# Optimization experiments

Measured on AMD Instinct MI355X. Metric: run time of the kernel, lower is better.

The kernel has to match this reference:

```python
import jax, jax.numpy as jnp
import numpy as np

A_COEF, B_COEF, C_COEF = 1.0, 0.1, 10.0
KL_COEF = 0.005
EPS = 1e-6

B, P1, F, P2 = 32, 778, 1538, 3000
PARAM_DIM, LATENT = 61, 64


def setup_inputs() -> dict:
    key = jax.random.key(0)
    ks = jax.random.split(key, 9)
    return {
        "recon_x": jax.random.normal(ks[0], (B, PARAM_DIM), jnp.float32),
        "x": jax.random.normal(ks[1], (B, PARAM_DIM), jnp.float32),
        "mu": jax.random.normal(ks[2], (B, LATENT), jnp.float32),
        "logvar": jax.random.normal(ks[3], (B, LATENT), jnp.float32),
        "recon_xyz": jax.random.normal(ks[4], (B, P1, 3), jnp.float32),
        "hand_xyz": jax.random.normal(ks[5], (B, P1, 3), jnp.float32),
        "hand_faces": jax.random.randint(ks[6], (B, F, 3), 0, P1, jnp.int64),
        "obj_pts": jax.random.normal(ks[7], (B, P2, 3), jnp.float32),
        "v_weights": jax.random.uniform(ks[8], (P1,), jnp.float32),
    }


def _verts_normals_single(verts, faces):
    # verts: (V,3), faces: (F,3). PyTorch3D-style area-weighted vertex normals.
    v0 = verts[faces[:, 0]]
    v1 = verts[faces[:, 1]]
    v2 = verts[faces[:, 2]]
    fn = jnp.cross(v1 - v0, v2 - v0)  # (F,3) ~ 2*area*face_normal
    n = (jnp.zeros_like(verts)
         .at[faces[:, 0]].add(fn)
         .at[faces[:, 1]].add(fn)
         .at[faces[:, 2]].add(fn))
    norm = jnp.linalg.norm(n, axis=-1, keepdims=True)
    return n / jnp.maximum(norm, EPS)


_verts_normals = jax.vmap(_verts_normals_single)


def _sqdist(xp, yp):
    # (B,P1,P2) pairwise squared distances
    x2 = jnp.sum(xp * xp, axis=-1)[:, :, None]
    y2 = jnp.sum(yp * yp, axis=-1)[:, None, :]
    return x2 + y2 - 2.0 * jnp.einsum('bpd,bqd->bpq', xp, yp)


def _point2point_signed(xp, yp, x_normals):
    # xp: (B,P1,3) hand, yp: (B,P2,3) object, x_normals: (B,P1,3)
    d2 = _sqdist(xp, yp)
    xidx = jnp.argmin(d2, axis=2)  # (B,P1) nearest object point per hand vert
    yidx = jnp.argmin(d2, axis=1)  # (B,P2) nearest hand vert per object point
    x_near = jnp.take_along_axis(yp, xidx[..., None], axis=1)  # (B,P1,3)
    y_near = jnp.take_along_axis(xp, yidx[..., None], axis=1)  # (B,P2,3)
    x2y = xp - x_near
    y2x = yp - y_near
    y_nn = jnp.take_along_axis(x_normals, yidx[..., None], axis=1)  # (B,P2,3)
    in_out = jnp.sign(jnp.sum(y_nn * y2x, axis=-1))
    y2x_signed = jnp.linalg.norm(y2x, axis=2) * in_out  # (B,P2)
    x2y_signed = jnp.linalg.norm(x2y, axis=2)           # (B,P1)
    return y2x_signed, x2y_signed


def _loss_cnet(verts_rhand, verts_rhand_gt, faces, verts_obj, v_weights):
    v_w2 = jnp.power(v_weights, 1.0 / 2.5)
    rh_n = _verts_normals(verts_rhand, faces)
    rh_n_gt = _verts_normals(verts_rhand_gt, faces)
    o2h, h2o = _point2point_signed(verts_rhand, verts_obj, rh_n)
    o2h_gt, h2o_gt = _point2point_signed(verts_rhand_gt, verts_obj, rh_n_gt)
    w_dist = (o2h_gt < 0.01) & (o2h_gt > -0.005)
    w_neg = o2h < 0.0
    w = jnp.where(w_neg, 1.5, jnp.where(w_dist, 1.0, 0.1))
    loss_h = 35.0 * (1.0 - KL_COEF) * jnp.mean(jnp.abs(jnp.abs(h2o) - jnp.abs(h2o_gt)) * v_w2)
    loss_o = 30.0 * (1.0 - KL_COEF) * jnp.mean(jnp.abs(o2h - o2h_gt) * w)
    return loss_h + loss_o


def reference(recon_x, x, mu, logvar, recon_xyz, hand_xyz, hand_faces, obj_pts, v_weights):
    bsz = recon_x.shape[0]
    param_loss = jnp.sum((recon_x - x) ** 2) / bsz
    recon_loss = jnp.sum((recon_xyz - hand_xyz) ** 2) / hand_xyz.shape[0]
    KLD = -0.5 * jnp.sum(1.0 + logvar - mu ** 2 - jnp.exp(logvar)) / hand_xyz.shape[0]
    cvae_loss = recon_loss + KLD
    ho_loss = _loss_cnet(recon_xyz, hand_xyz, hand_faces, obj_pts, v_weights)
    loss = A_COEF * cvae_loss + B_COEF * param_loss + C_COEF * ho_loss
    return loss, param_loss, ho_loss, recon_loss, KLD
```

## Files before the change

### kernel.cpp

```cpp
#include <hip/hip_runtime.h>
#include <math.h>

#define B 32
#define P1 778
#define NF 1538
#define P2 3000
#define PARAM_DIM 61
#define LATENT 64

#define P1PAD 784
#define NTH 49
#define CHO 768
#define NTO 12
#define NPART 16

#define RED1_BLKS 16
#define HC_BLKS 128
#define OC_BLKS 192
#define HALF_F 769

#define D1_NRM 128
#define D1_TOT (D1_NRM + RED1_BLKS)
#define D2_TOT 256
#define D3_TOT (OC_BLKS + HC_BLKS)

#define NP_OFF  0
#define NP_SZ   (2*2*B*P1*4)
#define OS_OFF  (NP_OFF + NP_SZ)
#define OS_SZ   (2*B*P2)
#define HP_OFF  (OS_OFF + OS_SZ)
#define HP_SZ   (NPART*2*B*P1PAD)
#define R1_OFF  (HP_OFF + HP_SZ)
#define RH_OFF  (R1_OFF + RED1_BLKS*3)
#define RO_OFF  (RH_OFF + HC_BLKS)

typedef __attribute__((ext_vector_type(8))) short bf16x8;
typedef __attribute__((ext_vector_type(4))) float f32x4;
union U4 { uint4 u; bf16x8 v; };

static __device__ __forceinline__ unsigned umin2(unsigned a, unsigned b) { return a < b ? a : b; }
static __device__ __forceinline__ unsigned bhi(float x) { return __float_as_uint(x) >> 16; }
static __device__ __forceinline__ float bres(float x, unsigned h) { return x - __uint_as_float(h << 16); }

__global__ __launch_bounds__(256) void kd1(
    const float* __restrict__ recon_x, const float* __restrict__ x,
    const float* __restrict__ mu, const float* __restrict__ logvar,
    const float* __restrict__ recon_xyz, const float* __restrict__ hand_xyz,
    const int* __restrict__ faces, float* __restrict__ ws) {
  __shared__ float4 sv[P1];
  __shared__ float sn[4][2336];
  const int tid = threadIdx.x;
  const int bid = blockIdx.x;

  if (bid < D1_NRM) {
    const int half = bid >> 6, r = bid & 63, set = r >> 5, b = r & 31;
    const float* verts = (set == 0 ? recon_xyz : hand_xyz) + b * P1 * 3;
    const int* f = faces + b * NF * 3 + half * HALF_F * 3;
    const int nf = (half == 0) ? HALF_F : (NF - HALF_F);
    for (int i = tid; i < P1; i += 256)
      sv[i] = make_float4(verts[3*i], verts[3*i+1], verts[3*i+2], 0.f);
    for (int i = tid; i < 4 * 2336; i += 256) ((float*)sn)[i] = 0.f;
    __syncthreads();
    float* s = sn[tid >> 6];
    for (int k = tid; k < nf; k += 256) {
      int i0 = f[3*k], i1 = f[3*k+1], i2 = f[3*k+2];
      float4 v0 = sv[i0], v1 = sv[i1], v2 = sv[i2];
      float e0x = v1.x - v0.x, e0y = v1.y - v0.y, e0z = v1.z - v0.z;
      float e1x = v2.x - v0.x, e1y = v2.y - v0.y, e1z = v2.z - v0.z;
      float fx = e0y * e1z - e0z * e1y;
      float fy = e0z * e1x - e0x * e1z;
      float fz = e0x * e1y - e0y * e1x;
      atomicAdd(&s[3*i0+0], fx); atomicAdd(&s[3*i0+1], fy); atomicAdd(&s[3*i0+2], fz);
      atomicAdd(&s[3*i1+0], fx); atomicAdd(&s[3*i1+1], fy); atomicAdd(&s[3*i1+2], fz);
      atomicAdd(&s[3*i2+0], fx); atomicAdd(&s[3*i2+1], fy); atomicAdd(&s[3*i2+2], fz);
    }
    __syncthreads();
    float4* np = (float4*)(ws + NP_OFF) + (size_t)((half * 2 + set) * B + b) * P1;
    for (int p = tid; p < P1; p += 256) {
      float nx = sn[0][3*p] + sn[1][3*p] + sn[2][3*p] + sn[3][3*p];
      float ny = sn[0][3*p+1] + sn[1][3*p+1] + sn[2][3*p+1] + sn[3][3*p+1];
      float nz = sn[0][3*p+2] + sn[1][3*p+2] + sn[2][3*p+2] + sn[3][3*p+2];
      np[p] = make_float4(nx, ny, nz, 0.f);
    }
  } else {
    const int blk = bid - D1_NRM;
    const int gtid = blk * 256 + tid, stride = RED1_BLKS * 256;
    float sp = 0.f, sr = 0.f, sk = 0.f;
    for (int i = gtid; i < B * PARAM_DIM; i += stride) { float d = recon_x[i] - x[i]; sp += d * d; }
    for (int i = gtid; i < B * P1 * 3; i += stride)    { float d = recon_xyz[i] - hand_xyz[i]; sr += d * d; }
    for (int i = gtid; i < B * LATENT; i += stride)    { float lv = logvar[i], m = mu[i]; sk += 1.f + lv - m * m - expf(lv); }
    for (int off = 32; off > 0; off >>= 1) {
      sp += __shfl_down(sp, off, 64);
      sr += __shfl_down(sr, off, 64);
      sk += __shfl_down(sk, off, 64);
    }
    float* sred = (float*)sn;
    const int wv = tid >> 6;
    if ((tid & 63) == 0) { sred[wv*3] = sp; sred[wv*3+1] = sr; sred[wv*3+2] = sk; }
    __syncthreads();
    if (tid == 0) {
      float a = 0.f, bb = 0.f, c = 0.f;
      for (int w = 0; w < 4; ++w) { a += sred[w*3]; bb += sred[w*3+1]; c += sred[w*3+2]; }
      ws[R1_OFF + blk*3+0] = a; ws[R1_OFF + blk*3+1] = bb; ws[R1_OFF + blk*3+2] = c;
    }
  }
}

__global__ __launch_bounds__(256, 1) void kd2(
    const float* __restrict__ recon_xyz, const float* __restrict__ hand_xyz,
    const float* __restrict__ obj, float* __restrict__ ws) {
  __shared__ float4 sVerts[P1PAD];
  __shared__ float4 sObj[CHO];
  __shared__ uint4  sPack4[(NTH + 1) * 32];
  __shared__ unsigned sKeys[CHO];
  __shared__ uint4  sZero;

  const int tid = threadIdx.x;
  const int bid = blockIdx.x;
  const int chunk = bid >> 6, rr = bid & 63, set = rr >> 5, b = rr & 31;
  const float* verts = (set == 0 ? recon_xyz : hand_xyz) + b * P1 * 3;
  const float* op = obj + (size_t)b * P2 * 3;

  if (tid == 0) sZero = make_uint4(0u, 0u, 0u, 0u);
  for (int i = tid; i < P1PAD; i += 256) {
    float vx, vy, vz;
    if (i < P1) { vx = verts[3*i]; vy = verts[3*i+1]; vz = verts[3*i+2]; }
    else        { vx = vy = vz = 1.0e6f; }
    sVerts[i] = make_float4(vx, vy, vz, 0.f);
  }
  for (int i = tid; i < CHO; i += 256) {
    const int q = chunk * CHO + i;
    float ox, oy, oz;
    if (q < P2) { ox = op[3*q]; oy = op[3*q+1]; oz = op[3*q+2]; }
    else        { ox = oy = oz = 1.0e6f; }
    sObj[i] = make_float4(ox, oy, oz, ox*ox + oy*oy + oz*oz);
  }
  __syncthreads();

  for (int idx = tid; idx < NTH * 32; idx += 256) {
    const int t = idx >> 5, vl = idx & 31, vg = vl >> 4;
    const float4 v = sVerts[t * 16 + (vl & 15)];
    const float sx = -2.f * v.x, sy = -2.f * v.y, sz = -2.f * v.z;
    const unsigned hx = bhi(sx), hy = bhi(sy), hz = bhi(sz);
    unsigned w0, w1, w2, w3;
    if (vg == 0) {
      const unsigned lx = bhi(bres(sx, hx));
      const unsigned ly = bhi(bres(sy, hy));
      const unsigned lz = bhi(bres(sz, hz));
      w0 = hx | (hy << 16);
      w1 = hz | (lx << 16);
      w2 = ly | (lz << 16);
      w3 = hx | (hy << 16);
    } else {
      const float h2 = v.x*v.x + v.y*v.y + v.z*v.z;
      const unsigned h2h = bhi(h2);
      const unsigned h2l = bhi(bres(h2, h2h));
      w0 = hz  | (h2h << 16);
      w1 = h2l | (0x3F80u << 16);
      w2 = 0x3F80u;
      w3 = 0u;
    }
    sPack4[t * 32 + vl] = make_uint4(w0, w1, w2, w3);
  }

  const int l = tid & 63, wv = tid >> 6, g = l >> 4, cl = l & 15;
  U4 bw[NTO];
  #pragma unroll
  for (int j = 0; j < NTO; ++j) {
    const float4 o = sObj[wv * 192 + j * 16 + cl];
    unsigned u0 = 0u, u1 = 0u, u2 = 0u, u3 = 0u;
    if (g == 0) {
      const unsigned ohx = bhi(o.x), ohy = bhi(o.y), ohz = bhi(o.z);
      const unsigned olx = bhi(bres(o.x, ohx));
      const unsigned oly = bhi(bres(o.y, ohy));
      u0 = ohx | (ohy << 16);
      u1 = ohz | (ohx << 16);
      u2 = ohy | (ohz << 16);
      u3 = olx | (oly << 16);
    } else if (g == 1) {
      const unsigned ohz = bhi(o.z);
      const unsigned olz = bhi(bres(o.z, ohz));
      const float o2p = o.w + 1.0f;
      const unsigned o2h = bhi(o2p);
      const unsigned o2l = bhi(bres(o2p, o2h));
      u0 = olz | (0x3F80u << 16);
      u1 = 0x3F80u | (o2h << 16);
      u2 = o2l;
      u3 = 0u;
    }
    bw[j].u = make_uint4(u0, u1, u2, u3);
  }
  __syncthreads();

  unsigned om[NTO];
  #pragma unroll
  for (int j = 0; j < NTO; ++j) om[j] = 0xFFFFFFFFu;

  float* hpart = ws + HP_OFF + (size_t)(((chunk * 4 + wv) * 2 + set) * B + b) * P1PAD;
  const f32x4 czero = {0.f, 0.f, 0.f, 0.f};

  const uint4* ap = (l < 32) ? ((const uint4*)sPack4 + l) : &sZero;
  const int astep = (l < 32) ? 32 : 0;
  uint4 au = *ap; ap += astep;

  int ib = g * 4;
  for (int t = 0; t < NTH; ++t, ib += 16) {
    const uint4 aunx = *ap; ap += astep;
    U4 ac; ac.u = au;
    float hm0 = 3.0e38f, hm1 = 3.0e38f, hm2 = 3.0e38f, hm3 = 3.0e38f;
    #pragma unroll
    for (int j = 0; j < NTO; ++j) {
      const f32x4 d = __builtin_amdgcn_mfma_f32_16x16x32_bf16(ac.v, bw[j].v, czero, 0, 0, 0);
      hm0 = fminf(hm0, d[0]); hm1 = fminf(hm1, d[1]);
      hm2 = fminf(hm2, d[2]); hm3 = fminf(hm3, d[3]);
      const unsigned k0 = (__float_as_uint(d[0]) & 0xFFFFFC00u) | (unsigned)(ib + 0);
      const unsigned k1 = (__float_as_uint(d[1]) & 0xFFFFFC00u) | (unsigned)(ib + 1);
      const unsigned k2 = (__float_as_uint(d[2]) & 0xFFFFFC00u) | (unsigned)(ib + 2);
      const unsigned k3 = (__float_as_uint(d[3]) & 0xFFFFFC00u) | (unsigned)(ib + 3);
      om[j] = umin2(om[j], umin2(umin2(k0, k1), umin2(k2, k3)));
    }
    #pragma unroll
    for (int m = 1; m <= 8; m <<= 1) {
      hm0 = fminf(hm0, __shfl_xor(hm0, m, 64));
      hm1 = fminf(hm1, __shfl_xor(hm1, m, 64));
      hm2 = fminf(hm2, __shfl_xor(hm2, m, 64));
      hm3 = fminf(hm3, __shfl_xor(hm3, m, 64));
    }
    if (cl == 0)
      *(float4*)&hpart[ib] = make_float4(hm0 - 1.f, hm1 - 1.f, hm2 - 1.f, hm3 - 1.f);
    au = aunx;
  }

  #pragma unroll
  for (int j = 0; j < NTO; ++j) {
    unsigned v = umin2(om[j], (unsigned)__shfl_xor((int)om[j], 16, 64));
    v = umin2(v, (unsigned)__shfl_xor((int)v, 32, 64));
    if (l < 16) sKeys[wv * 192 + j * 16 + l] = v;
  }
  __syncthreads();

  const float4* np0 = (const float4*)(ws + NP_OFF) + (size_t)(set * B + b) * P1;
  const float4* np1 = np0 + (size_t)2 * B * P1;
  float* os = ws + OS_OFF + (size_t)(set * B + b) * P2;
  for (int i = tid; i < CHO; i += 256) {
    const int q = chunk * CHO + i;
    if (q < P2) {
      const unsigned key = sKeys[i];
      int hi = (int)(key & 1023u); if (hi > P1 - 1) hi = P1 - 1;
      const float4 h = sVerts[hi];
      const float4 o = sObj[i];
      const float dx = o.x - h.x, dy = o.y - h.y, dz = o.z - h.z;
      const float d2 = fmaf(dx, dx, fmaf(dy, dy, dz * dz));
      const float4 na = np0[hi], nb = np1[hi];
      const float nx = na.x + nb.x, ny = na.y + nb.y, nz = na.z + nb.z;
      const float dt = nx * dx + ny * dy + nz * dz;
      const float sg = (dt > 0.f) ? 1.f : ((dt < 0.f) ? -1.f : 0.f);
      os[q] = sqrtf(d2) * sg;
    }
  }
}

__global__ __launch_bounds__(256) void kd3(const float* __restrict__ vw,
                                           float* __restrict__ ws) {
  __shared__ float sred[4];
  const int tid = threadIdx.x;
  const int bid = blockIdx.x;
  if (bid < OC_BLKS) {
    const int gtid = bid * 256 + tid, stride = OC_BLKS * 256;
    float so = 0.f;
    for (int i = gtid; i < B * P2; i += stride) {
      float osA = ws[OS_OFF + i];
      float osB = ws[OS_OFF + (size_t)B * P2 + i];
      bool wdist = (osB < 0.01f) && (osB > -0.005f);
      float w = (osA < 0.f) ? 1.5f : (wdist ? 1.f : 0.1f);
      so += fabsf(osA - osB) * w;
    }
    for (int off = 32; off > 0; off >>= 1) so += __shfl_down(so, off, 64);
    if ((tid & 63) == 0) sred[tid >> 6] = so;
    __syncthreads();
    if (tid == 0) ws[RO_OFF + bid] = sred[0] + sred[1] + sred[2] + sred[3];
  } else {
    const int blk = bid - OC_BLKS;
    const int gtid = blk * 256 + tid, stride = HC_BLKS * 256;
    float sh = 0.f;
    for (int i = gtid; i < B * P1; i += stride) {
      const int p = i % P1, bb = i / P1;
      const size_t base0 = (size_t)HP_OFF + (size_t)bb * P1PAD + p;
      float m0 = 3.0e38f, m1 = 3.0e38f;
      #pragma unroll
      for (int c = 0; c < NPART; ++c) {
        m0 = fminf(m0, ws[base0 + (size_t)(c*2+0) * B * P1PAD]);
        m1 = fminf(m1, ws[base0 + (size_t)(c*2+1) * B * P1PAD]);
      }
      m0 = fmaxf(m0, 0.f); m1 = fmaxf(m1, 0.f);
      sh += fabsf(sqrtf(m0) - sqrtf(m1)) * powf(vw[p], 0.4f);
    }
    for (int off = 32; off > 0; off >>= 1) sh += __shfl_down(sh, off, 64);
    if ((tid & 63) == 0) sred[tid >> 6] = sh;
    __syncthreads();
    if (tid == 0) ws[RH_OFF + blk] = sred[0] + sred[1] + sred[2] + sred[3];
  }
}

__global__ void kfin(const float* __restrict__ ws, float* __restrict__ out) {
  const int lane = threadIdx.x;
  float sp = 0.f, sr = 0.f, sk = 0.f, sh = 0.f, so = 0.f;
  for (int i = lane; i < RED1_BLKS; i += 64) {
    sp += ws[R1_OFF + i*3+0]; sr += ws[R1_OFF + i*3+1]; sk += ws[R1_OFF + i*3+2];
  }
  for (int i = lane; i < HC_BLKS; i += 64) sh += ws[RH_OFF + i];
  for (int i = lane; i < OC_BLKS; i += 64) so += ws[RO_OFF + i];
  for (int off = 32; off > 0; off >>= 1) {
    sp += __shfl_down(sp, off, 64);
    sr += __shfl_down(sr, off, 64);
    sk += __shfl_down(sk, off, 64);
    sh += __shfl_down(sh, off, 64);
    so += __shfl_down(so, off, 64);
  }
  if (lane == 0) {
    float param_loss = sp / (float)B;
    float recon_loss = sr / (float)B;
    float KLD = -0.5f * sk / (float)B;
    float cvae = recon_loss + KLD;
    float loss_h = 35.f * (1.f - 0.005f) * sh / (float)(B * P1);
    float loss_o = 30.f * (1.f - 0.005f) * so / (float)(B * P2);
    float ho = loss_h + loss_o;
    out[0] = cvae + 0.1f * param_loss + 10.f * ho;
    out[1] = param_loss;
    out[2] = ho;
    out[3] = recon_loss;
    out[4] = KLD;
  }
}

extern "C" void kernel_launch(void* const* d_in, const int* in_sizes, int n_in,
                              void* d_out, int out_size, void* d_ws, size_t ws_size,
                              hipStream_t stream) {
  const float* recon_x   = (const float*)d_in[0];
  const float* x         = (const float*)d_in[1];
  const float* mu        = (const float*)d_in[2];
  const float* logvar    = (const float*)d_in[3];
  const float* recon_xyz = (const float*)d_in[4];
  const float* hand_xyz  = (const float*)d_in[5];
  const int*   faces     = (const int*)d_in[6];
  const float* obj       = (const float*)d_in[7];
  const float* vw        = (const float*)d_in[8];
  float* ws = (float*)d_ws;
  float* out = (float*)d_out;

  kd1<<<dim3(D1_TOT), 256, 0, stream>>>(recon_x, x, mu, logvar,
                                        recon_xyz, hand_xyz, faces, ws);
  kd2<<<dim3(D2_TOT), 256, 0, stream>>>(recon_xyz, hand_xyz, obj, ws);
  kd3<<<dim3(D3_TOT), 256, 0, stream>>>(vw, ws);
  kfin<<<1, 64, 0, stream>>>(ws, out);
}
```

Baseline: 137.6 us.

## Split kd2 work so each wave covers a strided subset of hand tiles

Each kd2 block now handles 192 object points instead of 768, so the grid grows to 16 chunks × 64. Within a block the four waves share the same object tile and each takes every fourth hand tile. Per-wave keys are merged in shared memory. The shared vertex array is dropped and vertices are read directly from global memory, which cuts LDS use enough to allow 4 blocks per CU. The hand partial-min layout changes to one slice per chunk (16 partials), matching NPART. The aim is more blocks and more occupancy at the cost of repeating hand packing per block and extra global vertex gathers.

Measured after the change: 124.1 us. 9.8% less time.

```diff
diff --git a/kernel.cpp b/kernel.cpp
--- a/kernel.cpp
+++ b/kernel.cpp
@@ -10,8 +10,9 @@
 
 #define P1PAD 784
 #define NTH 49
-#define CHO 768
+#define CHO 192
 #define NTO 12
+#define NCH 16
 #define NPART 16
 
 #define RED1_BLKS 16
@@ -21,7 +22,7 @@
 
 #define D1_NRM 128
 #define D1_TOT (D1_NRM + RED1_BLKS)
-#define D2_TOT 256
+#define D2_TOT (NCH * 64)
 #define D3_TOT (OC_BLKS + HC_BLKS)
 
 #define NP_OFF  0
@@ -106,13 +107,12 @@
   }
 }
 
-__global__ __launch_bounds__(256, 1) void kd2(
+__global__ __launch_bounds__(256, 4) void kd2(
     const float* __restrict__ recon_xyz, const float* __restrict__ hand_xyz,
     const float* __restrict__ obj, float* __restrict__ ws) {
-  __shared__ float4 sVerts[P1PAD];
   __shared__ float4 sObj[CHO];
-  __shared__ uint4  sPack4[(NTH + 1) * 32];
-  __shared__ unsigned sKeys[CHO];
+  __shared__ uint4  sPack4[(NTH + 4) * 32];
+  __shared__ unsigned sKeys[4][CHO];
   __shared__ uint4  sZero;
 
   const int tid = threadIdx.x;
@@ -122,12 +122,6 @@
   const float* op = obj + (size_t)b * P2 * 3;
 
   if (tid == 0) sZero = make_uint4(0u, 0u, 0u, 0u);
-  for (int i = tid; i < P1PAD; i += 256) {
-    float vx, vy, vz;
-    if (i < P1) { vx = verts[3*i]; vy = verts[3*i+1]; vz = verts[3*i+2]; }
-    else        { vx = vy = vz = 1.0e6f; }
-    sVerts[i] = make_float4(vx, vy, vz, 0.f);
-  }
   for (int i = tid; i < CHO; i += 256) {
     const int q = chunk * CHO + i;
     float ox, oy, oz;
@@ -135,12 +129,13 @@
     else        { ox = oy = oz = 1.0e6f; }
     sObj[i] = make_float4(ox, oy, oz, ox*ox + oy*oy + oz*oz);
   }
-  __syncthreads();
-
   for (int idx = tid; idx < NTH * 32; idx += 256) {
     const int t = idx >> 5, vl = idx & 31, vg = vl >> 4;
-    const float4 v = sVerts[t * 16 + (vl & 15)];
-    const float sx = -2.f * v.x, sy = -2.f * v.y, sz = -2.f * v.z;
+    const int i = t * 16 + (vl & 15);
+    float vx, vy, vz;
+    if (i < P1) { vx = verts[3*i]; vy = verts[3*i+1]; vz = verts[3*i+2]; }
+    else        { vx = vy = vz = 1.0e6f; }
+    const float sx = -2.f * vx, sy = -2.f * vy, sz = -2.f * vz;
     const unsigned hx = bhi(sx), hy = bhi(sy), hz = bhi(sz);
     unsigned w0, w1, w2, w3;
     if (vg == 0) {
@@ -152,7 +147,7 @@
       w2 = ly | (lz << 16);
       w3 = hx | (hy << 16);
     } else {
-      const float h2 = v.x*v.x + v.y*v.y + v.z*v.z;
+      const float h2 = vx*vx + vy*vy + vz*vz;
       const unsigned h2h = bhi(h2);
       const unsigned h2l = bhi(bres(h2, h2h));
       w0 = hz  | (h2h << 16);
@@ -162,12 +157,13 @@
     }
     sPack4[t * 32 + vl] = make_uint4(w0, w1, w2, w3);
   }
+  __syncthreads();
 
   const int l = tid & 63, wv = tid >> 6, g = l >> 4, cl = l & 15;
   U4 bw[NTO];
   #pragma unroll
   for (int j = 0; j < NTO; ++j) {
-    const float4 o = sObj[wv * 192 + j * 16 + cl];
+    const float4 o = sObj[j * 16 + cl];
     unsigned u0 = 0u, u1 = 0u, u2 = 0u, u3 = 0u;
     if (g == 0) {
       const unsigned ohx = bhi(o.x), ohy = bhi(o.y), ohz = bhi(o.z);
@@ -190,21 +186,21 @@
     }
     bw[j].u = make_uint4(u0, u1, u2, u3);
   }
-  __syncthreads();
 
   unsigned om[NTO];
   #pragma unroll
   for (int j = 0; j < NTO; ++j) om[j] = 0xFFFFFFFFu;
 
-  float* hpart = ws + HP_OFF + (size_t)(((chunk * 4 + wv) * 2 + set) * B + b) * P1PAD;
+  float* hpart = ws + HP_OFF + (size_t)(((chunk * 2) + set) * B + b) * P1PAD;
   const f32x4 czero = {0.f, 0.f, 0.f, 0.f};
-
-  const uint4* ap = (l < 32) ? ((const uint4*)sPack4 + l) : &sZero;
-  const int astep = (l < 32) ? 32 : 0;
+  const int nt = (NTH - wv + 3) >> 2;
+
+  const uint4* ap = (l < 32) ? ((const uint4*)sPack4 + wv * 32 + l) : &sZero;
+  const int astep = (l < 32) ? 4 * 32 : 0;
   uint4 au = *ap; ap += astep;
 
-  int ib = g * 4;
-  for (int t = 0; t < NTH; ++t, ib += 16) {
+  for (int s = 0; s < nt; ++s) {
+    const int ib = (wv + 4 * s) * 16 + g * 4;
     const uint4 aunx = *ap; ap += astep;
     U4 ac; ac.u = au;
     float hm0 = 3.0e38f, hm1 = 3.0e38f, hm2 = 3.0e38f, hm3 = 3.0e38f;
@@ -235,7 +231,7 @@
   for (int j = 0; j < NTO; ++j) {
     unsigned v = umin2(om[j], (unsigned)__shfl_xor((int)om[j], 16, 64));
     v = umin2(v, (unsigned)__shfl_xor((int)v, 32, 64));
-    if (l < 16) sKeys[wv * 192 + j * 16 + l] = v;
+    if (l < 16) sKeys[wv][j * 16 + l] = v;
   }
   __syncthreads();
 
@@ -245,11 +241,12 @@
   for (int i = tid; i < CHO; i += 256) {
     const int q = chunk * CHO + i;
     if (q < P2) {
-      const unsigned key = sKeys[i];
+      const unsigned key = umin2(umin2(sKeys[0][i], sKeys[1][i]),
+                                 umin2(sKeys[2][i], sKeys[3][i]));
       int hi = (int)(key & 1023u); if (hi > P1 - 1) hi = P1 - 1;
-      const float4 h = sVerts[hi];
+      const float hx = verts[3*hi], hy = verts[3*hi+1], hz = verts[3*hi+2];
       const float4 o = sObj[i];
-      const float dx = o.x - h.x, dy = o.y - h.y, dz = o.z - h.z;
+      const float dx = o.x - hx, dy = o.y - hy, dz = o.z - hz;
       const float d2 = fmaf(dx, dx, fmaf(dy, dy, dz * dz));
       const float4 na = np0[hi], nb = np1[hi];
       const float nx = na.x + nb.x, ny = na.y + nb.y, nz = na.z + nb.z;
```
